# Kernel tuning notes

Hardware: AMD Instinct MI355X
Metric: run time of the kernel (lower is better)

## Reference

```python
import jax, jax.numpy as jnp
import numpy as np

B, S, D = 4, 512, 256
NTOPO = 8
LN_EPS = 1e-5


def _topo_features(xb):
    """Topology features for one batch element xb: [S, D] -> [8]."""
    # pairwise distances (torch.norm with subgradient 0 at zero)
    diffs = xb[:, None, :] - xb[None, :, :]          # [S, S, D]
    sq = jnp.sum(diffs * diffs, axis=-1)             # [S, S]
    pos = sq > 0
    dists = jnp.where(pos, jnp.sqrt(jnp.where(pos, sq, 1.0)), 0.0)

    # torch .median() returns the lower median: sorted[(n-1)//2]
    n = S * S
    thr = jnp.sort(dists.reshape(-1))[(n - 1) // 2]

    eye = jnp.eye(S, dtype=dists.dtype)
    connected = (dists < thr).astype(dists.dtype) * (1.0 - eye)  # [S, S]
    conn_ratio = connected.sum() / max(S * (S - 1), 1)

    # connected components via min-label propagation (== BFS component count)
    adj = jax.lax.stop_gradient(connected > 0)

    def step(lab):
        nbr_min = jnp.min(jnp.where(adj, lab[None, :], S), axis=1)
        return jnp.minimum(lab, nbr_min)

    labels = jax.lax.while_loop(lambda l: jnp.any(step(l) != l), step,
                                jnp.arange(S, dtype=jnp.int32))
    n_components = jnp.sum(labels == jnp.arange(S, dtype=jnp.int32)).astype(dists.dtype)

    avg_degree = connected.sum(axis=1).mean()

    # upper triangle INCLUDING diagonal (torch.triu default), masked reductions
    mask = jnp.triu(jnp.ones((S, S), dtype=bool))
    cnt = S * (S + 1) // 2
    dist_mean = jnp.sum(jnp.where(mask, dists, 0.0)) / cnt
    var = jnp.sum(jnp.where(mask, (dists - dist_mean) ** 2, 0.0)) / (cnt - 1)  # ddof=1
    dist_std = jnp.sqrt(var)
    dist_min = jnp.min(jnp.where(mask, dists, jnp.inf))
    dist_max = jnp.max(jnp.where(mask, dists, -jnp.inf))

    return jnp.stack([conn_ratio,
                      n_components / max(S, 1),
                      avg_degree / max(S, 1),
                      dist_mean, dist_std, dist_min, dist_max,
                      jnp.asarray(0.0, dists.dtype)])


def _layer_norm(h, gamma, beta):
    mu = jnp.mean(h, axis=-1, keepdims=True)
    var = jnp.mean((h - mu) ** 2, axis=-1, keepdims=True)
    return (h - mu) / jnp.sqrt(var + LN_EPS) * gamma + beta


def setup_inputs() -> dict:
    key = jax.random.key(0)
    k1, k2, k3 = jax.random.split(key, 3)
    x = jax.random.normal(k1, (B, S, D), dtype=jnp.float32)
    # nn.Linear(8, D): weight [D, 8], bias [D]
    bound = 1.0 / np.sqrt(NTOPO)
    W = jax.random.uniform(k2, (D, NTOPO), minval=-bound, maxval=bound, dtype=jnp.float32)
    b = jax.random.uniform(k3, (D,), minval=-bound, maxval=bound, dtype=jnp.float32)
    gamma = jnp.ones((D,), dtype=jnp.float32)
    beta = jnp.zeros((D,), dtype=jnp.float32)
    return {"x": x, "W": W, "b": b, "gamma": gamma, "beta": beta}


def reference(x, W, b, gamma, beta):
    topo = jax.vmap(_topo_features)(x)               # [B, 8]
    signal = topo @ W.T + b                          # [B, D]
    return _layer_norm(x + signal[:, None, :], gamma, beta)  # [B, S, D]
```

## Files before the change

### kernel.cpp

```cpp
#include <hip/hip_runtime.h>
#include <math.h>

#define SDIM 512
#define DDIM 256
#define NBATCH 4
#define SSQ (SDIM*SDIM)
#define MED_K ((SSQ-1)/2)
#define NBINS 4096
#define HLO 16.0f
#define HSCALE 256.0f
#define HINV (1.0f/256.0f)
#define PADK 264

#define OFF_DISTS   0ull
#define OFF_XBF     (2ull<<20)
#define OFF_NORMS   (6ull<<20)
#define OFF_HIST    ((6ull<<20) + 8192ull)
#define OFF_STATS   ((6ull<<20) + 40960ull)
#define OFF_SIGNAL  ((6ull<<20) + 41088ull)
#define OFF_ADJ     ((6ull<<20) + 45184ull)
#define NZERO ((32768 + 128) / 4)

typedef __attribute__((ext_vector_type(8))) short short8_t;
typedef __attribute__((ext_vector_type(4))) float f32x4_t;

__device__ __forceinline__ unsigned short f2bf(float f) {
    unsigned u = __float_as_uint(f);
    return (unsigned short)((u + 0x7FFFu + ((u >> 16) & 1u)) >> 16);
}

__global__ __launch_bounds__(256) void k_prep(const float* __restrict__ x,
                                              unsigned short* __restrict__ xbf,
                                              float* __restrict__ norms,
                                              unsigned* __restrict__ z) {
    const int tid = threadIdx.x;
    const int idx = blockIdx.x * 256 + tid;
    if (idx < NZERO) z[idx] = 0u;
    const int row = blockIdx.x * 4 + (tid >> 6);
    const int lane = tid & 63;
    const float4 v = *(const float4*)(x + (size_t)row * DDIM + lane * 4);
    float s = v.x * v.x + v.y * v.y + v.z * v.z + v.w * v.w;
#pragma unroll
    for (int off = 32; off; off >>= 1) s += __shfl_xor(s, off);
    ushort4 p = { f2bf(v.x), f2bf(v.y), f2bf(v.z), f2bf(v.w) };
    *(ushort4*)(xbf + (size_t)row * DDIM + lane * 4) = p;
    if (lane == 0) norms[row] = s;
}

__global__ __launch_bounds__(256) void k_dist(const unsigned short* __restrict__ xbf,
                                              const float* __restrict__ gnorms,
                                              unsigned short* __restrict__ udists,
                                              unsigned* __restrict__ ghist) {
    const int b  = blockIdx.z;
    const int i0 = blockIdx.y * 64, j0 = blockIdx.x * 64;
    __shared__ __align__(16) unsigned short Ab[64 * PADK];
    __shared__ __align__(16) unsigned short Bb[64 * PADK];
    __shared__ unsigned lh[NBINS / 2];
    __shared__ float nA[64], nB[64];
    const int tid = threadIdx.x;
    const unsigned short* xb = xbf + (size_t)b * SDIM * DDIM;

    for (int t = tid; t < NBINS / 2; t += 256) lh[t] = 0u;

    {
        const int r = tid >> 2, sub = tid & 3;
        const unsigned short* arow = xb + (size_t)(i0 + r) * DDIM + sub * 64;
        const unsigned short* brow = xb + (size_t)(j0 + r) * DDIM + sub * 64;
#pragma unroll
        for (int q = 0; q < 8; ++q) {
            *(short8_t*)&Ab[r * PADK + sub * 64 + q * 8] = *(const short8_t*)(arow + q * 8);
            *(short8_t*)&Bb[r * PADK + sub * 64 + q * 8] = *(const short8_t*)(brow + q * 8);
        }
    }
    if (tid < 64)                nA[tid]       = gnorms[(size_t)b * SDIM + i0 + tid];
    else if (tid < 128)          nB[tid - 64]  = gnorms[(size_t)b * SDIM + j0 + tid - 64];
    __syncthreads();

    const int w = tid >> 6, l = tid & 63;
    const int lrow = l & 15, lkb = l >> 4;
    f32x4_t ac0 = {0.f, 0.f, 0.f, 0.f}, ac1 = ac0, ac2 = ac0, ac3 = ac0;
    const unsigned short* Ap  = &Ab[(w * 16 + lrow) * PADK + lkb * 8];
    const unsigned short* Bp0 = &Bb[(0  + lrow) * PADK + lkb * 8];
    const unsigned short* Bp1 = &Bb[(16 + lrow) * PADK + lkb * 8];
    const unsigned short* Bp2 = &Bb[(32 + lrow) * PADK + lkb * 8];
    const unsigned short* Bp3 = &Bb[(48 + lrow) * PADK + lkb * 8];
#pragma unroll
    for (int ks = 0; ks < 8; ++ks) {
        short8_t af = *(const short8_t*)(Ap  + ks * 32);
        short8_t b0 = *(const short8_t*)(Bp0 + ks * 32);
        short8_t b1 = *(const short8_t*)(Bp1 + ks * 32);
        short8_t b2 = *(const short8_t*)(Bp2 + ks * 32);
        short8_t b3 = *(const short8_t*)(Bp3 + ks * 32);
        ac0 = __builtin_amdgcn_mfma_f32_16x16x32_bf16(af, b0, ac0, 0, 0, 0);
        ac1 = __builtin_amdgcn_mfma_f32_16x16x32_bf16(af, b1, ac1, 0, 0, 0);
        ac2 = __builtin_amdgcn_mfma_f32_16x16x32_bf16(af, b2, ac2, 0, 0, 0);
        ac3 = __builtin_amdgcn_mfma_f32_16x16x32_bf16(af, b3, ac3, 0, 0, 0);
    }

    unsigned short* udb = udists + (size_t)b * SSQ;
    const int orow = w * 16 + lkb * 4;
#pragma unroll
    for (int c = 0; c < 4; ++c) {
        const f32x4_t a = (c == 0) ? ac0 : (c == 1) ? ac1 : (c == 2) ? ac2 : ac3;
        const int jl = c * 16 + lrow;
        const float njv = nB[jl];
        const int gj = j0 + jl;
#pragma unroll
        for (int reg = 0; reg < 4; ++reg) {
            const int il = orow + reg;
            const int gi = i0 + il;
            float sq = fmaf(-2.0f, a[reg], nA[il] + njv);
            float d  = sq > 0.f ? sqrtf(sq) : 0.f;
            if (gi == gj) d = 0.f;
            int bin = (int)((d - HLO) * HSCALE);
            bin = bin < 0 ? 0 : (bin > (NBINS - 1) ? (NBINS - 1) : bin);
            udb[(size_t)gi * SDIM + gj] = (unsigned short)bin;
            atomicAdd(&lh[bin >> 1], (bin & 1) ? (1u << 16) : 1u);
        }
    }
    __syncthreads();
    unsigned* gh = ghist + (size_t)b * (NBINS / 2);
    for (int t = tid; t < NBINS / 2; t += 256) {
        unsigned v = lh[t];
        if (v) atomicAdd(&gh[t], v);
    }
}

__global__ __launch_bounds__(256) void k_adj(const unsigned short* __restrict__ ud,
                                             const unsigned* __restrict__ ghist,
                                             unsigned long long* __restrict__ adj,
                                             double* __restrict__ stats) {
    const int b = blockIdx.y, tid = threadIdx.x;
    const int w = tid >> 6, lane = tid & 63;
    const unsigned* h = ghist + (size_t)b * (NBINS / 2);
    unsigned lcnt[16];
    unsigned local = 0;
    float fsum = 0.f, fsq = 0.f;
    int mxb = -1;
#pragma unroll
    for (int qq = 0; qq < 8; ++qq) {
        unsigned pw = h[tid * 8 + qq];
        lcnt[2 * qq]     = pw & 0xffffu;
        lcnt[2 * qq + 1] = pw >> 16;
        local += lcnt[2 * qq] + lcnt[2 * qq + 1];
    }
#pragma unroll
    for (int t = 0; t < 16; ++t) {
        if (lcnt[t]) {
            const float mid = HLO + ((float)(tid * 16 + t) + 0.5f) * HINV;
            fsum += (float)lcnt[t] * mid;
            fsq  += (float)lcnt[t] * mid * mid;
            mxb = tid * 16 + t;
        }
    }
    unsigned inc = local;
#pragma unroll
    for (int off = 1; off < 64; off <<= 1) {
        unsigned v = __shfl_up(inc, off);
        if (lane >= off) inc += v;
    }
#pragma unroll
    for (int off = 32; off; off >>= 1) {
        fsum += __shfl_xor(fsum, off);
        fsq  += __shfl_xor(fsq, off);
        mxb   = max(mxb, __shfl_xor(mxb, off));
    }
    __shared__ unsigned wtot[4];
    __shared__ float wfs[4], wfq[4];
    __shared__ int wmx[4];
    __shared__ unsigned sbucket;
    if (lane == 63) wtot[w] = inc;
    if (lane == 0) { wfs[w] = fsum; wfq[w] = fsq; wmx[w] = mxb; }
    __syncthreads();
    unsigned woff = 0;
#pragma unroll
    for (int k = 0; k < 4; ++k) if (k < w) woff += wtot[k];
    const unsigned excl = inc + woff - local;
    if (MED_K >= excl && MED_K < excl + local) {
        unsigned run = excl;
        int bucket = tid * 16;
        for (int t = 0; t < 16; ++t) {
            if (MED_K < run + lcnt[t]) { bucket = tid * 16 + t; break; }
            run += lcnt[t];
        }
        sbucket = (unsigned)bucket;
    }
    if (tid == 0) {
        const float mid0 = HLO + 0.5f * HINV;
        double S = (double)(wfs[0] + wfs[1] + wfs[2] + wfs[3]) - 512.0 * (double)mid0;
        double Q = (double)(wfq[0] + wfq[1] + wfq[2] + wfq[3]) - 512.0 * (double)mid0 * mid0;
        int MX = max(max(wmx[0], wmx[1]), max(wmx[2], wmx[3]));
        double* st = stats + (size_t)b * 4;
        st[0] = S * 0.5;
        st[1] = Q * 0.5;
        ((unsigned*)st)[4] = __float_as_uint(HLO + ((float)MX + 0.5f) * HINV);
    }
    __syncthreads();
    const unsigned bucket = sbucket;

    const int i = blockIdx.x * 4 + w;
    const unsigned short* row = ud + (size_t)b * SSQ + (size_t)i * SDIM;
    int conn = 0;
    unsigned long long words[8];
#pragma unroll
    for (int c = 0; c < 8; ++c) {
        const int j = c * 64 + lane;
        const bool pred = (row[j] < bucket) && (j != i);
        words[c] = __ballot(pred ? 1 : 0);
        conn += pred ? 1 : 0;
    }
    if (lane == 0) {
#pragma unroll
        for (int c = 0; c < 8; ++c) adj[((size_t)b * SDIM + i) * 8 + c] = words[c];
    }
#pragma unroll
    for (int off = 32; off; off >>= 1) conn += __shfl_xor(conn, off);
    __shared__ int sh_c[4];
    if (lane == 0) sh_c[w] = conn;
    __syncthreads();
    if (tid == 0) {
        unsigned C0 = (unsigned)(sh_c[0] + sh_c[1] + sh_c[2] + sh_c[3]);
        atomicAdd(((unsigned*)(stats + (size_t)b * 4 + 2)) + 1, C0);
    }
}

__global__ __launch_bounds__(512) void k_ccsig(const uint4* __restrict__ adj,
                                               const double* __restrict__ stats,
                                               const float* __restrict__ W,
                                               const float* __restrict__ bias,
                                               float* __restrict__ signal) {
    const int b = blockIdx.x;
    __shared__ uint4 am[SDIM][4];
    __shared__ unsigned frontW[16], reachW[16];
    __shared__ int s_next, s_ncomp, s_any;
    const int tid = threadIdx.x;
    const uint4* ab = adj + (size_t)b * SDIM * 4;
    for (int t = tid; t < SDIM * 4; t += 512) ((uint4*)am)[t] = ab[t];
    if (tid < 16) { frontW[tid] = 0u; reachW[tid] = 0u; }
    if (tid == 0) s_ncomp = 0;
    __syncthreads();

    bool myReached = false;
    for (int comp = 0; comp < SDIM; ++comp) {
        if (tid == 0) {
            int s = -1;
            for (int w = 0; w < 16 && s < 0; ++w) {
                unsigned m = ~reachW[w];
                if (m) s = w * 32 + __ffs(m) - 1;
            }
            s_next = s;
            if (s >= 0) s_ncomp++;
        }
        __syncthreads();
        const int s = s_next;
        if (s < 0) break;
        if (tid < 16) {
            unsigned f = (tid == (s >> 5)) ? (1u << (s & 31)) : 0u;
            frontW[tid] = f;
            reachW[tid] |= f;
        }
        if (tid == s) myReached = true;
        __syncthreads();

        for (int it = 0; it < SDIM; ++it) {
            const uint4 f0 = *(const uint4*)&frontW[0];
            const uint4 f1 = *(const uint4*)&frontW[4];
            const uint4 f2 = *(const uint4*)&frontW[8];
            const uint4 f3 = *(const uint4*)&frontW[12];
            const uint4 r0 = am[tid][0], r1 = am[tid][1];
            const uint4 r2 = am[tid][2], r3 = am[tid][3];
            const unsigned inter =
                (r0.x & f0.x) | (r0.y & f0.y) | (r0.z & f0.z) | (r0.w & f0.w) |
                (r1.x & f1.x) | (r1.y & f1.y) | (r1.z & f1.z) | (r1.w & f1.w) |
                (r2.x & f2.x) | (r2.y & f2.y) | (r2.z & f2.z) | (r2.w & f2.w) |
                (r3.x & f3.x) | (r3.y & f3.y) | (r3.z & f3.z) | (r3.w & f3.w);
            const bool act = (inter != 0u) && !myReached;
            const unsigned long long bal = __ballot(act ? 1 : 0);
            __syncthreads();
            if ((tid & 63) == 0) {
                const int wv = tid >> 6;
                frontW[wv * 2]     = (unsigned)bal;
                frontW[wv * 2 + 1] = (unsigned)(bal >> 32);
            }
            if (tid == 0) s_any = 0;
            __syncthreads();
            if (act) myReached = true;
            if (tid < 16) {
                unsigned nf = frontW[tid];
                reachW[tid] |= nf;
                if (nf) atomicOr(&s_any, 1);
            }
            __syncthreads();
            if (!s_any) break;
        }
    }
    __syncthreads();

    if (tid < DDIM) {
        const double* st = stats + (size_t)b * 4;
        const unsigned* sw = (const unsigned*)st;
        const double sum = st[0], sumsq = st[1];
        const unsigned maxbits = sw[4], conn = sw[5];
        const double cntf = (double)(SDIM * (SDIM + 1) / 2);
        const double mean = sum / cntf;
        double var = (sumsq - sum * sum / cntf) / (cntf - 1.0);
        var = var > 0.0 ? var : 0.0;
        const float t0 = (float)((double)conn / (double)(SDIM * (SDIM - 1)));
        const float t1 = (float)s_ncomp / (float)SDIM;
        const float t2 = (float)((double)conn / (double)(SDIM * SDIM));
        const float t3 = (float)mean;
        const float t4 = (float)sqrt(var);
        const float t6 = __uint_as_float(maxbits);
        const float* w = W + tid * 8;
        signal[b * DDIM + tid] = bias[tid] + t0 * w[0] + t1 * w[1] + t2 * w[2]
                               + t3 * w[3] + t4 * w[4] + t6 * w[6];
    }
}

__global__ __launch_bounds__(256) void k_ln(const float* __restrict__ x,
                                            const float* __restrict__ signal,
                                            const float* __restrict__ gamma,
                                            const float* __restrict__ beta,
                                            float* __restrict__ out) {
    const int tid = threadIdx.x;
    const int w = tid >> 6, lane = tid & 63;
    const int row = blockIdx.x * 4 + w;
    const int b = row >> 9;
    const float4 xv = *(const float4*)(x + (size_t)row * DDIM + lane * 4);
    const float4 sg = *(const float4*)(signal + (size_t)b * DDIM + lane * 4);
    float h0 = xv.x + sg.x, h1 = xv.y + sg.y, h2 = xv.z + sg.z, h3 = xv.w + sg.w;
    float s = h0 + h1 + h2 + h3;
#pragma unroll
    for (int off = 32; off; off >>= 1) s += __shfl_xor(s, off);
    const float mu = s * (1.0f / 256.0f);
    const float d0 = h0 - mu, d1 = h1 - mu, d2 = h2 - mu, d3 = h3 - mu;
    float q = d0 * d0 + d1 * d1 + d2 * d2 + d3 * d3;
#pragma unroll
    for (int off = 32; off; off >>= 1) q += __shfl_xor(q, off);
    const float var = q * (1.0f / 256.0f);
    const float r = 1.0f / sqrtf(var + 1e-5f);
    const float4 g  = *(const float4*)(gamma + lane * 4);
    const float4 be = *(const float4*)(beta + lane * 4);
    float4 o;
    o.x = d0 * r * g.x + be.x;
    o.y = d1 * r * g.y + be.y;
    o.z = d2 * r * g.z + be.z;
    o.w = d3 * r * g.w + be.w;
    *(float4*)(out + (size_t)row * DDIM + lane * 4) = o;
}

extern "C" void kernel_launch(void* const* d_in, const int* in_sizes, int n_in,
                              void* d_out, int out_size, void* d_ws, size_t ws_size,
                              hipStream_t stream) {
    (void)in_sizes; (void)n_in; (void)out_size; (void)ws_size;
    const float* x     = (const float*)d_in[0];
    const float* W     = (const float*)d_in[1];
    const float* bias  = (const float*)d_in[2];
    const float* gamma = (const float*)d_in[3];
    const float* beta  = (const float*)d_in[4];
    float* out = (float*)d_out;

    char* ws = (char*)d_ws;
    unsigned short* udists = (unsigned short*)(ws + OFF_DISTS);
    unsigned short* xbf    = (unsigned short*)(ws + OFF_XBF);
    float*    norms  = (float*)(ws + OFF_NORMS);
    unsigned* ghist  = (unsigned*)(ws + OFF_HIST);
    double*   stats  = (double*)(ws + OFF_STATS);
    float*    signal = (float*)(ws + OFF_SIGNAL);
    unsigned long long* adj = (unsigned long long*)(ws + OFF_ADJ);

    k_prep  <<<512,                  256, 0, stream>>>(x, xbf, norms, (unsigned*)(ws + OFF_HIST));
    k_dist  <<<dim3(8, 8, NBATCH),   256, 0, stream>>>(xbf, norms, udists, ghist);
    k_adj   <<<dim3(128, NBATCH),    256, 0, stream>>>(udists, ghist, adj, stats);
    k_ccsig <<<NBATCH,               512, 0, stream>>>((const uint4*)adj, stats, W, bias, signal);
    k_ln    <<<512,                  256, 0, stream>>>(x, signal, gamma, beta, out);
}
```

Measured before the change: 34.92 us.

## Fuse median threshold and adjacency build into connected-components kernel

Merges the k_adj kernel into the per-batch connected-components kernel. Each of the 4 blocks now computes the median bucket from the histogram, builds the adjacency bitmask directly into shared memory, and keeps the stats in shared memory. This removes one launch and the global round-trip for the adjacency and stats buffers. In exchange, the 512x512 distance-bin scan now runs on only 4 blocks instead of 512, which serialises about 512KB of reads per block.

```diff
diff --git a/kernel.cpp b/kernel.cpp
--- a/kernel.cpp
+++ b/kernel.cpp
@@ -16,10 +16,8 @@
 #define OFF_XBF     (2ull<<20)
 #define OFF_NORMS   (6ull<<20)
 #define OFF_HIST    ((6ull<<20) + 8192ull)
-#define OFF_STATS   ((6ull<<20) + 40960ull)
-#define OFF_SIGNAL  ((6ull<<20) + 41088ull)
-#define OFF_ADJ     ((6ull<<20) + 45184ull)
-#define NZERO ((32768 + 128) / 4)
+#define OFF_SIGNAL  ((6ull<<20) + 40960ull)
+#define NZERO (32768 / 4)
 
 typedef __attribute__((ext_vector_type(8))) short short8_t;
 typedef __attribute__((ext_vector_type(4))) float f32x4_t;
@@ -126,118 +124,118 @@
     }
 }
 
-__global__ __launch_bounds__(256) void k_adj(const unsigned short* __restrict__ ud,
-                                             const unsigned* __restrict__ ghist,
-                                             unsigned long long* __restrict__ adj,
-                                             double* __restrict__ stats) {
-    const int b = blockIdx.y, tid = threadIdx.x;
-    const int w = tid >> 6, lane = tid & 63;
-    const unsigned* h = ghist + (size_t)b * (NBINS / 2);
-    unsigned lcnt[16];
-    unsigned local = 0;
-    float fsum = 0.f, fsq = 0.f;
-    int mxb = -1;
-#pragma unroll
-    for (int qq = 0; qq < 8; ++qq) {
-        unsigned pw = h[tid * 8 + qq];
-        lcnt[2 * qq]     = pw & 0xffffu;
-        lcnt[2 * qq + 1] = pw >> 16;
-        local += lcnt[2 * qq] + lcnt[2 * qq + 1];
-    }
-#pragma unroll
-    for (int t = 0; t < 16; ++t) {
-        if (lcnt[t]) {
-            const float mid = HLO + ((float)(tid * 16 + t) + 0.5f) * HINV;
-            fsum += (float)lcnt[t] * mid;
-            fsq  += (float)lcnt[t] * mid * mid;
-            mxb = tid * 16 + t;
-        }
-    }
-    unsigned inc = local;
-#pragma unroll
-    for (int off = 1; off < 64; off <<= 1) {
-        unsigned v = __shfl_up(inc, off);
-        if (lane >= off) inc += v;
-    }
-#pragma unroll
-    for (int off = 32; off; off >>= 1) {
-        fsum += __shfl_xor(fsum, off);
-        fsq  += __shfl_xor(fsq, off);
-        mxb   = max(mxb, __shfl_xor(mxb, off));
-    }
+__global__ __launch_bounds__(512) void k_medccsig(const unsigned short* __restrict__ ud,
+                                                  const unsigned* __restrict__ ghist,
+                                                  const float* __restrict__ W,
+                                                  const float* __restrict__ bias,
+                                                  float* __restrict__ signal) {
+    const int b = blockIdx.x;
+    __shared__ uint4 am[SDIM][4];
+    __shared__ unsigned frontW[16], reachW[16];
+    __shared__ int s_next, s_ncomp, s_any;
     __shared__ unsigned wtot[4];
     __shared__ float wfs[4], wfq[4];
     __shared__ int wmx[4];
     __shared__ unsigned sbucket;
-    if (lane == 63) wtot[w] = inc;
-    if (lane == 0) { wfs[w] = fsum; wfq[w] = fsq; wmx[w] = mxb; }
-    __syncthreads();
-    unsigned woff = 0;
-#pragma unroll
-    for (int k = 0; k < 4; ++k) if (k < w) woff += wtot[k];
-    const unsigned excl = inc + woff - local;
-    if (MED_K >= excl && MED_K < excl + local) {
-        unsigned run = excl;
-        int bucket = tid * 16;
+    __shared__ double s_sum, s_sumsq;
+    __shared__ float s_maxd;
+    __shared__ int wconn[8], s_conn;
+    const int tid = threadIdx.x;
+    const int wv = tid >> 6, lane = tid & 63;
+
+    unsigned lcnt[16];
+    unsigned local = 0, inc = 0;
+    if (tid < 256) {
+        const unsigned* h = ghist + (size_t)b * (NBINS / 2);
+        float fsum = 0.f, fsq = 0.f;
+        int mxb = -1;
+#pragma unroll
+        for (int qq = 0; qq < 8; ++qq) {
+            unsigned pw = h[tid * 8 + qq];
+            lcnt[2 * qq]     = pw & 0xffffu;
+            lcnt[2 * qq + 1] = pw >> 16;
+            local += lcnt[2 * qq] + lcnt[2 * qq + 1];
+        }
+#pragma unroll
         for (int t = 0; t < 16; ++t) {
-            if (MED_K < run + lcnt[t]) { bucket = tid * 16 + t; break; }
-            run += lcnt[t];
-        }
-        sbucket = (unsigned)bucket;
+            if (lcnt[t]) {
+                const float mid = HLO + ((float)(tid * 16 + t) + 0.5f) * HINV;
+                fsum += (float)lcnt[t] * mid;
+                fsq  += (float)lcnt[t] * mid * mid;
+                mxb = tid * 16 + t;
+            }
+        }
+        inc = local;
+#pragma unroll
+        for (int off = 1; off < 64; off <<= 1) {
+            unsigned v = __shfl_up(inc, off);
+            if (lane >= off) inc += v;
+        }
+#pragma unroll
+        for (int off = 32; off; off >>= 1) {
+            fsum += __shfl_xor(fsum, off);
+            fsq  += __shfl_xor(fsq, off);
+            mxb   = max(mxb, __shfl_xor(mxb, off));
+        }
+        if (lane == 63) wtot[wv] = inc;
+        if (lane == 0) { wfs[wv] = fsum; wfq[wv] = fsq; wmx[wv] = mxb; }
+    }
+    if (tid < 16) { frontW[tid] = 0u; reachW[tid] = 0u; }
+    if (tid == 0) s_ncomp = 0;
+    __syncthreads();
+    if (tid < 256) {
+        unsigned woff = 0;
+#pragma unroll
+        for (int k = 0; k < 4; ++k) if (k < wv) woff += wtot[k];
+        const unsigned excl = inc + woff - local;
+        if (MED_K >= excl && MED_K < excl + local) {
+            unsigned run = excl;
+            int bucket = tid * 16;
+            for (int t = 0; t < 16; ++t) {
+                if (MED_K < run + lcnt[t]) { bucket = tid * 16 + t; break; }
+                run += lcnt[t];
+            }
+            sbucket = (unsigned)bucket;
+        }
     }
     if (tid == 0) {
         const float mid0 = HLO + 0.5f * HINV;
-        double S = (double)(wfs[0] + wfs[1] + wfs[2] + wfs[3]) - 512.0 * (double)mid0;
-        double Q = (double)(wfq[0] + wfq[1] + wfq[2] + wfq[3]) - 512.0 * (double)mid0 * mid0;
+        s_sum   = ((double)(wfs[0] + wfs[1] + wfs[2] + wfs[3]) - 512.0 * (double)mid0) * 0.5;
+        s_sumsq = ((double)(wfq[0] + wfq[1] + wfq[2] + wfq[3]) - 512.0 * (double)mid0 * mid0) * 0.5;
         int MX = max(max(wmx[0], wmx[1]), max(wmx[2], wmx[3]));
-        double* st = stats + (size_t)b * 4;
-        st[0] = S * 0.5;
-        st[1] = Q * 0.5;
-        ((unsigned*)st)[4] = __float_as_uint(HLO + ((float)MX + 0.5f) * HINV);
+        s_maxd  = HLO + ((float)MX + 0.5f) * HINV;
     }
     __syncthreads();
     const unsigned bucket = sbucket;
 
-    const int i = blockIdx.x * 4 + w;
-    const unsigned short* row = ud + (size_t)b * SSQ + (size_t)i * SDIM;
-    int conn = 0;
-    unsigned long long words[8];
-#pragma unroll
-    for (int c = 0; c < 8; ++c) {
-        const int j = c * 64 + lane;
-        const bool pred = (row[j] < bucket) && (j != i);
-        words[c] = __ballot(pred ? 1 : 0);
-        conn += pred ? 1 : 0;
-    }
-    if (lane == 0) {
-#pragma unroll
-        for (int c = 0; c < 8; ++c) adj[((size_t)b * SDIM + i) * 8 + c] = words[c];
-    }
-#pragma unroll
-    for (int off = 32; off; off >>= 1) conn += __shfl_xor(conn, off);
-    __shared__ int sh_c[4];
-    if (lane == 0) sh_c[w] = conn;
+    {
+        const unsigned short* udb = ud + (size_t)b * SSQ;
+        int connl = 0;
+        for (int pass = 0; pass < 64; ++pass) {
+            const int i = wv * 64 + pass;
+            const unsigned short* row = udb + (size_t)i * SDIM;
+            unsigned long long wbits[8];
+#pragma unroll
+            for (int c = 0; c < 8; ++c) {
+                const int j = c * 64 + lane;
+                const bool pred = (row[j] < bucket) && (j != i);
+                wbits[c] = __ballot(pred ? 1 : 0);
+            }
+            if (lane == 0) {
+                unsigned long long* amr = (unsigned long long*)&am[i][0];
+#pragma unroll
+                for (int c = 0; c < 8; ++c) { amr[c] = wbits[c]; connl += __popcll(wbits[c]); }
+            }
+        }
+        if (lane == 0) wconn[wv] = connl;
+    }
     __syncthreads();
     if (tid == 0) {
-        unsigned C0 = (unsigned)(sh_c[0] + sh_c[1] + sh_c[2] + sh_c[3]);
-        atomicAdd(((unsigned*)(stats + (size_t)b * 4 + 2)) + 1, C0);
-    }
-}
-
-__global__ __launch_bounds__(512) void k_ccsig(const uint4* __restrict__ adj,
-                                               const double* __restrict__ stats,
-                                               const float* __restrict__ W,
-                                               const float* __restrict__ bias,
-                                               float* __restrict__ signal) {
-    const int b = blockIdx.x;
-    __shared__ uint4 am[SDIM][4];
-    __shared__ unsigned frontW[16], reachW[16];
-    __shared__ int s_next, s_ncomp, s_any;
-    const int tid = threadIdx.x;
-    const uint4* ab = adj + (size_t)b * SDIM * 4;
-    for (int t = tid; t < SDIM * 4; t += 512) ((uint4*)am)[t] = ab[t];
-    if (tid < 16) { frontW[tid] = 0u; reachW[tid] = 0u; }
-    if (tid == 0) s_ncomp = 0;
+        int cc = 0;
+#pragma unroll
+        for (int k = 0; k < 8; ++k) cc += wconn[k];
+        s_conn = cc;
+    }
     __syncthreads();
 
     bool myReached = false;
@@ -278,7 +276,6 @@
             const unsigned long long bal = __ballot(act ? 1 : 0);
             __syncthreads();
             if ((tid & 63) == 0) {
-                const int wv = tid >> 6;
                 frontW[wv * 2]     = (unsigned)bal;
                 frontW[wv * 2 + 1] = (unsigned)(bal >> 32);
             }
@@ -297,10 +294,8 @@
     __syncthreads();
 
     if (tid < DDIM) {
-        const double* st = stats + (size_t)b * 4;
-        const unsigned* sw = (const unsigned*)st;
-        const double sum = st[0], sumsq = st[1];
-        const unsigned maxbits = sw[4], conn = sw[5];
+        const double sum = s_sum, sumsq = s_sumsq;
+        const unsigned conn = (unsigned)s_conn;
         const double cntf = (double)(SDIM * (SDIM + 1) / 2);
         const double mean = sum / cntf;
         double var = (sumsq - sum * sum / cntf) / (cntf - 1.0);
@@ -310,7 +305,7 @@
         const float t2 = (float)((double)conn / (double)(SDIM * SDIM));
         const float t3 = (float)mean;
         const float t4 = (float)sqrt(var);
-        const float t6 = __uint_as_float(maxbits);
+        const float t6 = s_maxd;
         const float* w = W + tid * 8;
         signal[b * DDIM + tid] = bias[tid] + t0 * w[0] + t1 * w[1] + t2 * w[2]
                                + t3 * w[3] + t4 * w[4] + t6 * w[6];
@@ -365,13 +360,10 @@
     unsigned short* xbf    = (unsigned short*)(ws + OFF_XBF);
     float*    norms  = (float*)(ws + OFF_NORMS);
     unsigned* ghist  = (unsigned*)(ws + OFF_HIST);
-    double*   stats  = (double*)(ws + OFF_STATS);
     float*    signal = (float*)(ws + OFF_SIGNAL);
-    unsigned long long* adj = (unsigned long long*)(ws + OFF_ADJ);
-
-    k_prep  <<<512,                  256, 0, stream>>>(x, xbf, norms, (unsigned*)(ws + OFF_HIST));
-    k_dist  <<<dim3(8, 8, NBATCH),   256, 0, stream>>>(xbf, norms, udists, ghist);
-    k_adj   <<<dim3(128, NBATCH),    256, 0, stream>>>(udists, ghist, adj, stats);
-    k_ccsig <<<NBATCH,               512, 0, stream>>>((const uint4*)adj, stats, W, bias, signal);
-    k_ln    <<<512,                  256, 0, stream>>>(x, signal, gamma, beta, out);
-}
+
+    k_prep     <<<512,                256, 0, stream>>>(x, xbf, norms, ghist);
+    k_dist     <<<dim3(8, 8, NBATCH), 256, 0, stream>>>(xbf, norms, udists, ghist);
+    k_medccsig <<<NBATCH,             512, 0, stream>>>(udists, ghist, W, bias, signal);
+    k_ln       <<<512,                256, 0, stream>>>(x, signal, gamma, beta, out);
+}
```

Result: slower. 60.91 us (+74.4%).
